# Kernel optimization log

Measured on AMD Instinct MI355X. Metric: run time of the kernel, lower is better.

The kernel has to match this reference:

```python
import jax, jax.numpy as jnp
import numpy as np

B, L, DIM = 2, 2048, 768
NH, HD = 12, 64  # num_heads, head_dim; NH*HD == dim_attn == 768


def setup_inputs() -> dict:
    key = jax.random.key(0)
    ks = jax.random.split(key, 7)
    x = jax.random.normal(ks[0], (B, L, DIM), dtype=jnp.float32)
    pos_bias = jax.random.normal(ks[1], (1, NH, L, L), dtype=jnp.float32)
    Wq = jax.random.normal(ks[2], (DIM, DIM), dtype=jnp.float32) * 0.02
    Wk = jax.random.normal(ks[3], (DIM, DIM), dtype=jnp.float32) * 0.02
    Wv = jax.random.normal(ks[4], (DIM, DIM), dtype=jnp.float32) * 0.02
    Wo = jax.random.normal(ks[5], (DIM, DIM), dtype=jnp.float32) * 0.02
    mask = jax.random.randint(ks[6], (B, L), 0, 2, dtype=jnp.int32)
    return {"x": x, "pos_bias": pos_bias, "Wq": Wq, "Wk": Wk, "Wv": Wv,
            "Wo": Wo, "mask": mask}


def reference(x, pos_bias, Wq, Wk, Wv, Wo, mask):
    b, l, _ = x.shape
    # q/k/v projections (torch Linear: x @ W.T), split into heads
    q = (x @ Wq.T).reshape(b, l, NH, HD)
    k = (x @ Wk.T).reshape(b, l, NH, HD)
    v = (x @ Wv.T).reshape(b, l, NH, HD)
    # additive bias [B, H, Lq, Lk]: pos_bias broadcast + key mask -> -inf
    neg_inf = jnp.finfo(x.dtype).min
    attn_bias = jnp.broadcast_to(pos_bias, (b, NH, l, l))
    attn_bias = jnp.where(mask[:, None, None, :] == 0, neg_inf, attn_bias)
    # T5-style attention: NO 1/sqrt(d) scaling
    scores = jnp.einsum('binc,bjnc->bnij', q, k) + attn_bias
    attn = jax.nn.softmax(scores.astype(jnp.float32), axis=-1).astype(x.dtype)
    out = jnp.einsum('bnij,bjnc->binc', attn, v).reshape(b, l, NH * HD)
    return out @ Wo.T
```

## Files before the change

### kernel.cpp

```cpp
#include <hip/hip_runtime.h>
#include <math.h>

#define Bq 2
#define Lq 2048
#define DIMq 768
#define NHq 12
#define HDq 64

typedef __attribute__((ext_vector_type(8))) short short8;
typedef __attribute__((ext_vector_type(4))) short short4v;
typedef __attribute__((ext_vector_type(4))) float float4v;

#define GL2LDS(g, l) __builtin_amdgcn_global_load_lds( \
    (const __attribute__((address_space(1))) unsigned int*)(g), \
    (__attribute__((address_space(3))) unsigned int*)(l), 16, 0, 0)

static __device__ __forceinline__ short f2bf(float f) {
    union { float f; unsigned u; } v; v.f = f;
    unsigned r = (v.u + 0x7FFF + ((v.u >> 16) & 1)) >> 16;
    return (short)r;
}

__global__ __launch_bounds__(256)
void to_bf16(const float* __restrict__ x,  const float* __restrict__ wq,
             const float* __restrict__ wk, const float* __restrict__ wv,
             const float* __restrict__ wo,
             short* __restrict__ xb, short* __restrict__ wqb,
             short* __restrict__ wkb, short* __restrict__ wvb,
             short* __restrict__ wob)
{
    int blk = blockIdx.x;
    const float* s; short* d; int off;
    if      (blk <  768) { s = x;  d = xb;  off = blk * 1024; }
    else if (blk <  912) { s = wq; d = wqb; off = (blk -  768) * 1024; }
    else if (blk < 1056) { s = wk; d = wkb; off = (blk -  912) * 1024; }
    else if (blk < 1200) { s = wv; d = wvb; off = (blk - 1056) * 1024; }
    else                 { s = wo; d = wob; off = (blk - 1200) * 1024; }
    const float4* s4 = (const float4*)s;
    short4v* d4 = (short4v*)d;
#pragma unroll
    for (int i = 0; i < 4; ++i) {
        int idx = off + threadIdx.x + i * 256;
        float4 v = s4[idx];
        short4v o;
        o[0] = f2bf(v.x); o[1] = f2bf(v.y); o[2] = f2bf(v.z); o[3] = f2bf(v.w);
        d4[idx] = o;
    }
}

__global__ __launch_bounds__(256, 2)
void gemm128(const short* __restrict__ A, const short* __restrict__ W,
             short* __restrict__ Qg, short* __restrict__ Ktg,
             short* __restrict__ Vtg, float* __restrict__ OutF, int mode)
{
    __shared__ __align__(16) short As[128 * 64];
    __shared__ __align__(16) short Bs[128 * 64];
    const int tid = threadIdx.x;
    const int wave = tid >> 6, lane = tid & 63;
    const int col = lane & 15, quad = lane >> 4;
    const int m0 = blockIdx.y * 128, n0 = blockIdx.x * 128;
    const int mw = (wave & 1) * 64, nw = (wave >> 1) * 64;
    const int lr8 = lane >> 3, lc8 = lane & 7;

    float4v acc[4][4];
#pragma unroll
    for (int it = 0; it < 4; ++it)
#pragma unroll
        for (int nt = 0; nt < 4; ++nt) acc[it][nt] = (float4v){0.f, 0.f, 0.f, 0.f};

    for (int k0 = 0; k0 < DIMq; k0 += 64) {
        if (k0) __syncthreads();
#pragma unroll
        for (int i = 0; i < 4; ++i) {
            int issue = wave * 4 + i;
            int r = issue * 8 + lr8;
            int c = lc8 ^ (r & 7);
            GL2LDS(A + (size_t)(m0 + r) * DIMq + k0 + c * 8, &As[issue * 512]);
            GL2LDS(W + (size_t)(n0 + r) * DIMq + k0 + c * 8, &Bs[issue * 512]);
        }
        __syncthreads();
#pragma unroll
        for (int kk = 0; kk < 2; ++kk) {
            short8 a[4], bfr[4];
#pragma unroll
            for (int it = 0; it < 4; ++it) {
                int r = mw + it * 16 + col;
                a[it] = *(const short8*)&As[r * 64 + (((kk * 4 + quad) ^ (r & 7)) * 8)];
            }
#pragma unroll
            for (int nt = 0; nt < 4; ++nt) {
                int r = nw + nt * 16 + col;
                bfr[nt] = *(const short8*)&Bs[r * 64 + (((kk * 4 + quad) ^ (r & 7)) * 8)];
            }
#pragma unroll
            for (int it = 0; it < 4; ++it)
#pragma unroll
                for (int nt = 0; nt < 4; ++nt)
                    acc[it][nt] = __builtin_amdgcn_mfma_f32_16x16x32_bf16(
                        a[it], bfr[nt], acc[it][nt], 0, 0, 0);
        }
    }

    if (mode == 0) {
#pragma unroll
        for (int it = 0; it < 4; ++it)
#pragma unroll
            for (int reg = 0; reg < 4; ++reg) {
                float* orow = OutF + (size_t)(m0 + mw + it * 16 + quad * 4 + reg) * DIMq
                            + n0 + nw + col;
#pragma unroll
                for (int nt = 0; nt < 4; ++nt) orow[nt * 16] = acc[it][nt][reg];
            }
    } else {
        const int mat = n0 / 768;
        const int nbase = n0 - mat * 768 + nw;
#pragma unroll
        for (int it = 0; it < 4; ++it)
#pragma unroll
            for (int reg = 0; reg < 4; ++reg) {
                int m = m0 + mw + it * 16 + quad * 4 + reg;
                int bb = m >> 11, l = m & 2047;
#pragma unroll
                for (int nt = 0; nt < 4; ++nt) {
                    int nloc = nbase + nt * 16 + col;
                    int hh = nloc >> 6, c = nloc & 63;
                    size_t bh = (size_t)(bb * NHq + hh);
                    short v = f2bf(acc[it][nt][reg]);
                    if (mat == 0) {
                        Qg[(bh * Lq + l) * HDq + c] = v;
                    } else if (mat == 1) {
                        Ktg[(bh * 64 + (l >> 5)) * 2048 + (l & 31) * 64
                            + (((c >> 3) ^ (l & 7)) * 8) + (c & 7)] = v;
                    } else {
                        Vtg[(bh * 64 + (l >> 5)) * 2048 + c * 32
                            + ((((l & 31) >> 3) + (c >> 1)) & 3) * 8 + (l & 7)] = v;
                    }
                }
            }
    }
}

__global__ __launch_bounds__(256, 3)
void attn_fwd2(const short* __restrict__ Qg, const short* __restrict__ Ktg,
               const short* __restrict__ Vtg, const float* __restrict__ pos_bias,
               const int* __restrict__ mask, short* __restrict__ AO)
{
    __shared__ __align__(16) short Ks[2][2048];
    __shared__ __align__(16) short Vt[2][2048];
    __shared__ __align__(16) float Bsh[2][2048];
    __shared__ __align__(16) float mAll[Lq];
    __shared__ __align__(16) short Ps[64][40];

    const int qt = blockIdx.x, h = blockIdx.y, b = blockIdx.z;
    const int bh = b * NHq + h;
    const int tid = threadIdx.x;
    const int wave = tid >> 6, lane = tid & 63;
    const int col = lane & 15, quad = lane >> 4;
    const int lr8 = lane >> 3, lc8 = lane & 7;

    const short* Kb = Ktg + (size_t)bh * 64 * 2048;
    const short* Vb = Vtg + (size_t)bh * 64 * 2048;
    const float* Bb = pos_bias + (size_t)h * Lq * Lq + (size_t)(qt * 64) * Lq;
    const int* mk = mask + b * Lq;

    for (int i = tid; i < Lq; i += 256) mAll[i] = mk[i] ? 0.0f : -1e38f;

    const short* qrow = Qg + ((size_t)bh * Lq + qt * 64 + wave * 16 + col) * HDq;
    const short8 qa0 = *(const short8*)&qrow[quad * 8];
    const short8 qa1 = *(const short8*)&qrow[32 + quad * 8];

    auto stage = [&](int kt, int buf) {
        GL2LDS(Kb + (size_t)kt * 2048 + wave * 512 + lane * 8, &Ks[buf][wave * 512]);
        GL2LDS(Vb + (size_t)kt * 2048 + wave * 512 + lane * 8, &Vt[buf][wave * 512]);
#pragma unroll
        for (int j2 = 0; j2 < 2; ++j2) {
            int j = wave * 2 + j2;
            GL2LDS(Bb + (size_t)(j * 8 + lr8) * Lq + kt * 32 + lc8 * 4,
                   &Bsh[buf][j * 256]);
        }
    };

    stage(0, 0);

    float4v O[4];
    float m_run[4], l_run[4];
#pragma unroll
    for (int nt = 0; nt < 4; ++nt) O[nt] = (float4v){0.f, 0.f, 0.f, 0.f};
#pragma unroll
    for (int r = 0; r < 4; ++r) { m_run[r] = -1e37f; l_run[r] = 0.f; }

    __syncthreads();

    const int brow = wave * 16 + quad * 4;
    for (int kt = 0; kt < 64; ++kt) {
        const int cur = kt & 1;
        if (kt + 1 < 64) stage(kt + 1, cur ^ 1);

        float4v S[2];
#pragma unroll
        for (int nt = 0; nt < 2; ++nt) {
            S[nt] = (float4v){0.f, 0.f, 0.f, 0.f};
            int key = nt * 16 + col;
            short8 kb0 = *(const short8*)&Ks[cur][key * 64 + ((quad ^ (key & 7)) * 8)];
            short8 kb1 = *(const short8*)&Ks[cur][key * 64 + (((4 + quad) ^ (key & 7)) * 8)];
            S[nt] = __builtin_amdgcn_mfma_f32_16x16x32_bf16(qa0, kb0, S[nt], 0, 0, 0);
            S[nt] = __builtin_amdgcn_mfma_f32_16x16x32_bf16(qa1, kb1, S[nt], 0, 0, 0);
        }

        float sc[2][4];
#pragma unroll
        for (int nt = 0; nt < 2; ++nt) {
            float fm = mAll[kt * 32 + col + 16 * nt];
#pragma unroll
            for (int reg = 0; reg < 4; ++reg)
                sc[nt][reg] = S[nt][reg] + Bsh[cur][(brow + reg) * 32 + col + 16 * nt] + fm;
        }
        float tm[4], alpha[4], ps[4];
#pragma unroll
        for (int reg = 0; reg < 4; ++reg) {
            tm[reg] = fmaxf(sc[0][reg], sc[1][reg]);
#pragma unroll
            for (int off = 1; off < 16; off <<= 1)
                tm[reg] = fmaxf(tm[reg], __shfl_xor(tm[reg], off, 64));
            float mn = fmaxf(m_run[reg], tm[reg]);
            alpha[reg] = __expf(m_run[reg] - mn);
            m_run[reg] = mn;
            ps[reg] = 0.f;
        }
#pragma unroll
        for (int nt = 0; nt < 2; ++nt)
#pragma unroll
            for (int reg = 0; reg < 4; ++reg) {
                float p = __expf(sc[nt][reg] - m_run[reg]);
                sc[nt][reg] = p;
                ps[reg] += p;
            }
#pragma unroll
        for (int reg = 0; reg < 4; ++reg) {
#pragma unroll
            for (int off = 1; off < 16; off <<= 1)
                ps[reg] += __shfl_xor(ps[reg], off, 64);
            l_run[reg] = l_run[reg] * alpha[reg] + ps[reg];
        }
#pragma unroll
        for (int nt = 0; nt < 2; ++nt)
#pragma unroll
            for (int reg = 0; reg < 4; ++reg)
                Ps[brow + reg][col + 16 * nt] = f2bf(sc[nt][reg]);
#pragma unroll
        for (int nt = 0; nt < 4; ++nt)
#pragma unroll
            for (int reg = 0; reg < 4; ++reg)
                O[nt][reg] *= alpha[reg];
        asm volatile("s_waitcnt lgkmcnt(0)" ::: "memory");

        short8 pa = *(const short8*)&Ps[wave * 16 + col][quad * 8];
#pragma unroll
        for (int nt = 0; nt < 4; ++nt) {
            int hd = nt * 16 + col;
            short8 vb = *(const short8*)&Vt[cur][hd * 32 + (((quad + (hd >> 1)) & 3) * 8)];
            O[nt] = __builtin_amdgcn_mfma_f32_16x16x32_bf16(pa, vb, O[nt], 0, 0, 0);
        }

        __syncthreads();
    }

    short* aorow = AO + ((size_t)b * Lq + qt * 64 + brow) * DIMq + h * HDq + col;
#pragma unroll
    for (int reg = 0; reg < 4; ++reg) {
        float inv = 1.0f / l_run[reg];
#pragma unroll
        for (int nt = 0; nt < 4; ++nt)
            aorow[(size_t)reg * DIMq + 16 * nt] = f2bf(O[nt][reg] * inv);
    }
}

extern "C" void kernel_launch(void* const* d_in, const int* in_sizes, int n_in,
                              void* d_out, int out_size, void* d_ws, size_t ws_size,
                              hipStream_t stream) {
    const float* x        = (const float*)d_in[0];
    const float* pos_bias = (const float*)d_in[1];
    const float* Wq       = (const float*)d_in[2];
    const float* Wk       = (const float*)d_in[3];
    const float* Wv       = (const float*)d_in[4];
    const float* Wo       = (const float*)d_in[5];
    const int*   mask     = (const int*)d_in[6];
    float* out = (float*)d_out;

    const size_t nX = (size_t)Bq * Lq * DIMq;
    const size_t nW = (size_t)DIMq * DIMq;
    short* xb   = (short*)d_ws;
    short* wqkv = xb + nX;
    short* wob  = wqkv + 3 * nW;
    short* Qg   = wob + nW;
    short* Ktg  = Qg + nX;
    short* Vtg  = Ktg + nX;
    short* AOb  = Vtg + nX;

    dim3 blk(256);
    hipLaunchKernelGGL(to_bf16, dim3(1344), blk, 0, stream,
                       x, Wq, Wk, Wv, Wo, xb, wqkv, wqkv + nW, wqkv + 2 * nW, wob);

    hipLaunchKernelGGL(gemm128, dim3(2304 / 128, (Bq * Lq) / 128), blk, 0, stream,
                       xb, wqkv, Qg, Ktg, Vtg, (float*)nullptr, 1);

    hipLaunchKernelGGL(attn_fwd2, dim3(Lq / 64, NHq, Bq), blk, 0, stream,
                       Qg, Ktg, Vtg, pos_bias, mask, AOb);

    hipLaunchKernelGGL(gemm128, dim3(DIMq / 128, (Bq * Lq) / 128), blk, 0, stream,
                       AOb, wob, (short*)nullptr, (short*)nullptr,
                       (short*)nullptr, out, 0);
}
```

Baseline: 431.9 us.

## Transpose attention MFMA operands so bias loads directly into registers

Swaps the MFMA operand order in the attention kernel so each lane owns a full query row. This turns the row max and sum reductions into two cross-quad shuffles and lets the pos_bias tile be prefetched straight from global into registers instead of staged through LDS. The V projection epilogue also computes a transposed tile and writes V with an XOR swizzle, and the P tile becomes per-wave packed bf16 writes. Dropping the bias LDS buffer allows higher occupancy (launch bounds 4 for attention, 3 for the GEMM), at the cost of register-held bias prefetch and uncoalesced-ish bias reads of 16 bytes per lane.

Measured after the change: 455.7 us. 1.06x slower.

```diff
diff --git a/kernel.cpp b/kernel.cpp
--- a/kernel.cpp
+++ b/kernel.cpp
@@ -19,6 +19,9 @@
     union { float f; unsigned u; } v; v.f = f;
     unsigned r = (v.u + 0x7FFF + ((v.u >> 16) & 1)) >> 16;
     return (short)r;
+}
+static __device__ __forceinline__ unsigned pack2bf(float a, float b) {
+    return (unsigned)(unsigned short)f2bf(a) | ((unsigned)(unsigned short)f2bf(b) << 16);
 }
 
 __global__ __launch_bounds__(256)
@@ -48,7 +51,7 @@
     }
 }
 
-__global__ __launch_bounds__(256, 2)
+__global__ __launch_bounds__(256, 3)
 void gemm128(const short* __restrict__ A, const short* __restrict__ W,
              short* __restrict__ Qg, short* __restrict__ Ktg,
              short* __restrict__ Vtg, float* __restrict__ OutF, int mode)
@@ -61,6 +64,7 @@
     const int m0 = blockIdx.y * 128, n0 = blockIdx.x * 128;
     const int mw = (wave & 1) * 64, nw = (wave >> 1) * 64;
     const int lr8 = lane >> 3, lc8 = lane & 7;
+    const bool trn = (mode == 1) && (n0 >= 1536);
 
     float4v acc[4][4];
 #pragma unroll
@@ -92,12 +96,21 @@
                 int r = nw + nt * 16 + col;
                 bfr[nt] = *(const short8*)&Bs[r * 64 + (((kk * 4 + quad) ^ (r & 7)) * 8)];
             }
-#pragma unroll
-            for (int it = 0; it < 4; ++it)
-#pragma unroll
-                for (int nt = 0; nt < 4; ++nt)
-                    acc[it][nt] = __builtin_amdgcn_mfma_f32_16x16x32_bf16(
-                        a[it], bfr[nt], acc[it][nt], 0, 0, 0);
+            if (trn) {
+#pragma unroll
+                for (int it = 0; it < 4; ++it)
+#pragma unroll
+                    for (int nt = 0; nt < 4; ++nt)
+                        acc[it][nt] = __builtin_amdgcn_mfma_f32_16x16x32_bf16(
+                            bfr[nt], a[it], acc[it][nt], 0, 0, 0);
+            } else {
+#pragma unroll
+                for (int it = 0; it < 4; ++it)
+#pragma unroll
+                    for (int nt = 0; nt < 4; ++nt)
+                        acc[it][nt] = __builtin_amdgcn_mfma_f32_16x16x32_bf16(
+                            a[it], bfr[nt], acc[it][nt], 0, 0, 0);
+            }
         }
     }
 
@@ -111,7 +124,7 @@
 #pragma unroll
                 for (int nt = 0; nt < 4; ++nt) orow[nt * 16] = acc[it][nt][reg];
             }
-    } else {
+    } else if (!trn) {
         const int mat = n0 / 768;
         const int nbase = n0 - mat * 768 + nw;
 #pragma unroll
@@ -128,39 +141,50 @@
                     short v = f2bf(acc[it][nt][reg]);
                     if (mat == 0) {
                         Qg[(bh * Lq + l) * HDq + c] = v;
-                    } else if (mat == 1) {
+                    } else {
                         Ktg[(bh * 64 + (l >> 5)) * 2048 + (l & 31) * 64
                             + (((c >> 3) ^ (l & 7)) * 8) + (c & 7)] = v;
-                    } else {
-                        Vtg[(bh * 64 + (l >> 5)) * 2048 + c * 32
-                            + ((((l & 31) >> 3) + (c >> 1)) & 3) * 8 + (l & 7)] = v;
                     }
                 }
             }
-    }
-}
-
-__global__ __launch_bounds__(256, 3)
-void attn_fwd2(const short* __restrict__ Qg, const short* __restrict__ Ktg,
+    } else {
+        const int nbase = n0 - 1536 + nw;
+#pragma unroll
+        for (int it = 0; it < 4; ++it)
+#pragma unroll
+            for (int nt = 0; nt < 4; ++nt)
+#pragma unroll
+                for (int reg = 0; reg < 4; ++reg) {
+                    int n = nbase + nt * 16 + quad * 4 + reg;
+                    int hh = n >> 6, c = n & 63;
+                    int t = m0 + mw + it * 16 + col;
+                    int bb = t >> 11, l = t & 2047;
+                    size_t bh = (size_t)(bb * NHq + hh);
+                    Vtg[(bh * 64 + (l >> 5)) * 2048 + c * 32
+                        + ((((l & 31) >> 3) ^ (c & 3)) * 8) + (l & 7)]
+                        = f2bf(acc[it][nt][reg]);
+                }
+    }
+}
+
+__global__ __launch_bounds__(256, 4)
+void attn_fwd3(const short* __restrict__ Qg, const short* __restrict__ Ktg,
                const short* __restrict__ Vtg, const float* __restrict__ pos_bias,
                const int* __restrict__ mask, short* __restrict__ AO)
 {
     __shared__ __align__(16) short Ks[2][2048];
     __shared__ __align__(16) short Vt[2][2048];
-    __shared__ __align__(16) float Bsh[2][2048];
     __shared__ __align__(16) float mAll[Lq];
-    __shared__ __align__(16) short Ps[64][40];
+    __shared__ __align__(16) short Ps[4][16][48];
 
     const int qt = blockIdx.x, h = blockIdx.y, b = blockIdx.z;
     const int bh = b * NHq + h;
     const int tid = threadIdx.x;
     const int wave = tid >> 6, lane = tid & 63;
     const int col = lane & 15, quad = lane >> 4;
-    const int lr8 = lane >> 3, lc8 = lane & 7;
 
     const short* Kb = Ktg + (size_t)bh * 64 * 2048;
     const short* Vb = Vtg + (size_t)bh * 64 * 2048;
-    const float* Bb = pos_bias + (size_t)h * Lq * Lq + (size_t)(qt * 64) * Lq;
     const int* mk = mask + b * Lq;
 
     for (int i = tid; i < Lq; i += 256) mAll[i] = mk[i] ? 0.0f : -1e38f;
@@ -169,109 +193,99 @@
     const short8 qa0 = *(const short8*)&qrow[quad * 8];
     const short8 qa1 = *(const short8*)&qrow[32 + quad * 8];
 
+    const float* Bb = pos_bias + (size_t)h * Lq * Lq
+                    + (size_t)(qt * 64 + wave * 16 + col) * Lq + quad * 4;
+
     auto stage = [&](int kt, int buf) {
         GL2LDS(Kb + (size_t)kt * 2048 + wave * 512 + lane * 8, &Ks[buf][wave * 512]);
         GL2LDS(Vb + (size_t)kt * 2048 + wave * 512 + lane * 8, &Vt[buf][wave * 512]);
-#pragma unroll
-        for (int j2 = 0; j2 < 2; ++j2) {
-            int j = wave * 2 + j2;
-            GL2LDS(Bb + (size_t)(j * 8 + lr8) * Lq + kt * 32 + lc8 * 4,
-                   &Bsh[buf][j * 256]);
-        }
     };
+    float4v bias_cur[2], bias_nxt[2];
+    auto pre_bias = [&](int kt, float4v (&bb)[2]) {
+#pragma unroll
+        for (int nt = 0; nt < 2; ++nt)
+            bb[nt] = *(const float4v*)&Bb[kt * 32 + nt * 16];
+    };
 
     stage(0, 0);
+    pre_bias(0, bias_cur);
 
     float4v O[4];
-    float m_run[4], l_run[4];
 #pragma unroll
     for (int nt = 0; nt < 4; ++nt) O[nt] = (float4v){0.f, 0.f, 0.f, 0.f};
-#pragma unroll
-    for (int r = 0; r < 4; ++r) { m_run[r] = -1e37f; l_run[r] = 0.f; }
+    float m_run = -1e37f, l_run = 0.f;
 
     __syncthreads();
 
-    const int brow = wave * 16 + quad * 4;
     for (int kt = 0; kt < 64; ++kt) {
         const int cur = kt & 1;
-        if (kt + 1 < 64) stage(kt + 1, cur ^ 1);
+        if (kt + 1 < 64) { stage(kt + 1, cur ^ 1); pre_bias(kt + 1, bias_nxt); }
 
         float4v S[2];
 #pragma unroll
         for (int nt = 0; nt < 2; ++nt) {
-            S[nt] = (float4v){0.f, 0.f, 0.f, 0.f};
+            float4v mb = *(const float4v*)&mAll[kt * 32 + nt * 16 + quad * 4];
+            S[nt] = bias_cur[nt] + mb;
             int key = nt * 16 + col;
             short8 kb0 = *(const short8*)&Ks[cur][key * 64 + ((quad ^ (key & 7)) * 8)];
             short8 kb1 = *(const short8*)&Ks[cur][key * 64 + (((4 + quad) ^ (key & 7)) * 8)];
-            S[nt] = __builtin_amdgcn_mfma_f32_16x16x32_bf16(qa0, kb0, S[nt], 0, 0, 0);
-            S[nt] = __builtin_amdgcn_mfma_f32_16x16x32_bf16(qa1, kb1, S[nt], 0, 0, 0);
-        }
-
-        float sc[2][4];
+            S[nt] = __builtin_amdgcn_mfma_f32_16x16x32_bf16(kb0, qa0, S[nt], 0, 0, 0);
+            S[nt] = __builtin_amdgcn_mfma_f32_16x16x32_bf16(kb1, qa1, S[nt], 0, 0, 0);
+        }
+
+        float tm = fmaxf(fmaxf(fmaxf(S[0][0], S[0][1]), fmaxf(S[0][2], S[0][3])),
+                         fmaxf(fmaxf(S[1][0], S[1][1]), fmaxf(S[1][2], S[1][3])));
+        tm = fmaxf(tm, __shfl_xor(tm, 16, 64));
+        tm = fmaxf(tm, __shfl_xor(tm, 32, 64));
+        float mnew = fmaxf(m_run, tm);
+        float alpha = __expf(m_run - mnew);
+        m_run = mnew;
+        float p[2][4], ps = 0.f;
+#pragma unroll
+        for (int nt = 0; nt < 2; ++nt)
+#pragma unroll
+            for (int reg = 0; reg < 4; ++reg) {
+                float pv = __expf(S[nt][reg] - mnew);
+                p[nt][reg] = pv;
+                ps += pv;
+            }
+        ps += __shfl_xor(ps, 16, 64);
+        ps += __shfl_xor(ps, 32, 64);
+        l_run = l_run * alpha + ps;
+
 #pragma unroll
         for (int nt = 0; nt < 2; ++nt) {
-            float fm = mAll[kt * 32 + col + 16 * nt];
+            *(unsigned*)&Ps[wave][col][nt * 16 + quad * 4]     = pack2bf(p[nt][0], p[nt][1]);
+            *(unsigned*)&Ps[wave][col][nt * 16 + quad * 4 + 2] = pack2bf(p[nt][2], p[nt][3]);
+        }
+#pragma unroll
+        for (int nt = 0; nt < 4; ++nt)
 #pragma unroll
             for (int reg = 0; reg < 4; ++reg)
-                sc[nt][reg] = S[nt][reg] + Bsh[cur][(brow + reg) * 32 + col + 16 * nt] + fm;
-        }
-        float tm[4], alpha[4], ps[4];
-#pragma unroll
-        for (int reg = 0; reg < 4; ++reg) {
-            tm[reg] = fmaxf(sc[0][reg], sc[1][reg]);
-#pragma unroll
-            for (int off = 1; off < 16; off <<= 1)
-                tm[reg] = fmaxf(tm[reg], __shfl_xor(tm[reg], off, 64));
-            float mn = fmaxf(m_run[reg], tm[reg]);
-            alpha[reg] = __expf(m_run[reg] - mn);
-            m_run[reg] = mn;
-            ps[reg] = 0.f;
-        }
-#pragma unroll
-        for (int nt = 0; nt < 2; ++nt)
-#pragma unroll
-            for (int reg = 0; reg < 4; ++reg) {
-                float p = __expf(sc[nt][reg] - m_run[reg]);
-                sc[nt][reg] = p;
-                ps[reg] += p;
-            }
-#pragma unroll
-        for (int reg = 0; reg < 4; ++reg) {
-#pragma unroll
-            for (int off = 1; off < 16; off <<= 1)
-                ps[reg] += __shfl_xor(ps[reg], off, 64);
-            l_run[reg] = l_run[reg] * alpha[reg] + ps[reg];
-        }
-#pragma unroll
-        for (int nt = 0; nt < 2; ++nt)
-#pragma unroll
-            for (int reg = 0; reg < 4; ++reg)
-                Ps[brow + reg][col + 16 * nt] = f2bf(sc[nt][reg]);
-#pragma unroll
-        for (int nt = 0; nt < 4; ++nt)
-#pragma unroll
-            for (int reg = 0; reg < 4; ++reg)
-                O[nt][reg] *= alpha[reg];
+                O[nt][reg] *= alpha;
         asm volatile("s_waitcnt lgkmcnt(0)" ::: "memory");
 
-        short8 pa = *(const short8*)&Ps[wave * 16 + col][quad * 8];
+        short8 pa = *(const short8*)&Ps[wave][col][quad * 8];
 #pragma unroll
         for (int nt = 0; nt < 4; ++nt) {
             int hd = nt * 16 + col;
-            short8 vb = *(const short8*)&Vt[cur][hd * 32 + (((quad + (hd >> 1)) & 3) * 8)];
-            O[nt] = __builtin_amdgcn_mfma_f32_16x16x32_bf16(pa, vb, O[nt], 0, 0, 0);
-        }
-
+            short8 vb = *(const short8*)&Vt[cur][hd * 32 + ((quad ^ (hd & 3)) * 8)];
+            O[nt] = __builtin_amdgcn_mfma_f32_16x16x32_bf16(vb, pa, O[nt], 0, 0, 0);
+        }
+
+#pragma unroll
+        for (int nt = 0; nt < 2; ++nt) bias_cur[nt] = bias_nxt[nt];
         __syncthreads();
     }
 
-    short* aorow = AO + ((size_t)b * Lq + qt * 64 + brow) * DIMq + h * HDq + col;
-#pragma unroll
-    for (int reg = 0; reg < 4; ++reg) {
-        float inv = 1.0f / l_run[reg];
-#pragma unroll
-        for (int nt = 0; nt < 4; ++nt)
-            aorow[(size_t)reg * DIMq + 16 * nt] = f2bf(O[nt][reg] * inv);
+    float inv = 1.0f / l_run;
+    short* ao = AO + ((size_t)b * Lq + qt * 64 + wave * 16 + col) * DIMq + h * HDq;
+#pragma unroll
+    for (int nt = 0; nt < 4; ++nt) {
+        short4v v4;
+#pragma unroll
+        for (int reg = 0; reg < 4; ++reg) v4[reg] = f2bf(O[nt][reg] * inv);
+        *(short4v*)&ao[nt * 16 + quad * 4] = v4;
     }
 }
 
@@ -304,7 +318,7 @@
     hipLaunchKernelGGL(gemm128, dim3(2304 / 128, (Bq * Lq) / 128), blk, 0, stream,
                        xb, wqkv, Qg, Ktg, Vtg, (float*)nullptr, 1);
 
-    hipLaunchKernelGGL(attn_fwd2, dim3(Lq / 64, NHq, Bq), blk, 0, stream,
+    hipLaunchKernelGGL(attn_fwd3, dim3(Lq / 64, NHq, Bq), blk, 0, stream,
                        Qg, Ktg, Vtg, pos_bias, mask, AOb);
 
     hipLaunchKernelGGL(gemm128, dim3(DIMq / 128, (Bq * Lq) / 128), blk, 0, stream,
```
